# Optimization experiments

Hardware: AMD Instinct MI355X
Metric: run time of the kernel (lower is better)

The kernel has to match this reference:

```python
import jax, jax.numpy as jnp
import numpy as np

STRIDE = 32
ANCHORS = np.array([[10, 13], [16, 30], [33, 23], [30, 61], [62, 45],
                    [59, 119], [116, 90], [156, 198], [373, 326]], np.float32)
ALL_ANCH = ANCHORS / STRIDE           # [9,2] anchor w,h in grid units
ANCH_MASK = [6, 7, 8]
MASKED_ANCH = ALL_ANCH[ANCH_MASK]     # [3,2]
N_CLASSES = 80
N_ANCHORS = 3
IGNORE_THRE = 0.5


def _bce_sum(p, t, w=1.0):
    # torch BCELoss(sum): clamps log terms at -100 to avoid 0*inf
    lp = jnp.maximum(jnp.log(p), -100.0)
    lq = jnp.maximum(jnp.log(1.0 - p), -100.0)
    return jnp.sum(-w * (t * lp + (1.0 - t) * lq))


def _iou_xywh(a, b):
    # a: [B,N,4], b: [B,K,4] in (cx,cy,w,h) -> IoU [B,N,K]
    tl = jnp.maximum(a[:, :, None, :2] - a[:, :, None, 2:] / 2,
                     b[:, None, :, :2] - b[:, None, :, 2:] / 2)
    br = jnp.minimum(a[:, :, None, :2] + a[:, :, None, 2:] / 2,
                     b[:, None, :, :2] + b[:, None, :, 2:] / 2)
    en = jnp.all(tl < br, axis=-1).astype(a.dtype)
    inter = jnp.prod(br - tl, axis=-1) * en
    area_a = a[:, :, 2] * a[:, :, 3]
    area_b = b[:, :, 2] * b[:, :, 3]
    return inter / (area_a[:, :, None] + area_b[:, None, :] - inter)


def setup_inputs() -> dict:
    key = jax.random.key(0)
    k1, k2, k3, k4 = jax.random.split(key, 4)
    B, M, F, A, NC = 128, 60, 19, 3, 80
    output = jax.random.normal(k1, (B, A * (5 + NC), F, F), jnp.float32)
    cxy = jax.random.uniform(k2, (B, M, 2), jnp.float32, 100.0, 500.0)
    wh = jax.random.uniform(k3, (B, M, 2), jnp.float32, 64.0, 192.0)
    cls = jax.random.randint(k4, (B, M, 1), 0, NC).astype(jnp.float32)
    labels = jnp.concatenate([cxy - wh / 2, cxy + wh / 2, cls], axis=-1)
    return {"output": output, "labels": labels}


def reference(output, labels):
    B = output.shape[0]
    F = output.shape[2]
    n_ch = 5 + N_CLASSES
    labels = jax.lax.stop_gradient(labels)  # torch detaches labels

    # [B, A, F, F, n_ch]; sigmoid on x,y,obj,cls; raw on w,h
    out = output.reshape(B, N_ANCHORS, n_ch, F, F).transpose(0, 1, 3, 4, 2)
    out = jnp.concatenate([jax.nn.sigmoid(out[..., :2]), out[..., 2:4],
                           jax.nn.sigmoid(out[..., 4:])], axis=-1)

    # decoded pred boxes (grid units), detached as in torch (.data)
    xs = jnp.arange(F, dtype=out.dtype)
    wa = jnp.asarray(MASKED_ANCH[:, 0])[None, :, None, None]
    ha = jnp.asarray(MASKED_ANCH[:, 1])[None, :, None, None]
    px = out[..., 0] + xs[None, None, None, :]
    py = out[..., 1] + xs[None, None, :, None]
    pw = jnp.exp(out[..., 2]) * wa
    ph = jnp.exp(out[..., 3]) * ha
    pred = jax.lax.stop_gradient(jnp.stack([px, py, pw, ph], axis=-1))

    valid = labels.sum(axis=2) > 0                               # [B,M]
    tx = jnp.floor(labels[..., 0] / STRIDE)
    ty = jnp.floor(labels[..., 1] / STRIDE)
    tw = jnp.floor((labels[..., 2] - labels[..., 0]) / STRIDE)
    th = jnp.floor((labels[..., 3] - labels[..., 1]) / STRIDE)
    ti = tx.astype(jnp.int32)
    tj = ty.astype(jnp.int32)

    # anchor matching: IoU of (0,0,w,h) truths vs (0,0,aw,ah) ref anchors
    ref_wh = jnp.asarray(ALL_ANCH)                               # [9,2]
    mw = jnp.minimum(tw[..., None], ref_wh[:, 0])
    mh = jnp.minimum(th[..., None], ref_wh[:, 1])
    en = ((mw > 0) & (mh > 0)).astype(out.dtype)
    inter = mw * mh * en
    aiou = inter / (tw[..., None] * th[..., None]
                    + ref_wh[:, 0] * ref_wh[:, 1] - inter)       # [B,M,9]
    best_all = jnp.argmax(aiou, axis=-1)                         # [B,M]
    best_n = best_all % 3
    best_mask = best_all >= ANCH_MASK[0]

    # ignore mask from pred-vs-truth IoU
    truth_box = jnp.stack([tx, ty, tw, th], axis=-1)             # [B,M,4]
    ious = _iou_xywh(pred.reshape(B, -1, 4), truth_box)          # [B,AFF,M]
    ious = ious * valid[:, None, :].astype(out.dtype)
    best_iou = ious.max(axis=-1)
    obj_mask = (best_iou <= IGNORE_THRE).astype(out.dtype).reshape(B, N_ANCHORS, F, F)

    # scatter matched truths into (b, a, j, i) cells
    matched = valid & best_mask                                  # [B,M]
    NT = B * N_ANCHORS * F * F
    b_idx = jnp.broadcast_to(jnp.arange(B, dtype=jnp.int32)[:, None], matched.shape)
    flat = ((b_idx * N_ANCHORS + best_n.astype(jnp.int32)) * F + tj) * F + ti
    flat = jnp.where(matched, flat, NT).reshape(-1)              # NT is OOB -> dropped

    obj_mask = obj_mask.reshape(-1).at[flat].set(1.0, mode='drop').reshape(B, N_ANCHORS, F, F)
    tgt_mask = jnp.zeros((NT, 4 + N_CLASSES), out.dtype).at[flat].set(1.0, mode='drop')
    tgt_mask = tgt_mask.reshape(B, N_ANCHORS, F, F, 4 + N_CLASSES)

    txf = tx - tx.astype(jnp.int32).astype(out.dtype)   # exactly 0 (as in torch)
    tyf = ty - ty.astype(jnp.int32).astype(out.dtype)
    anch = jnp.asarray(MASKED_ANCH)[best_n]                      # [B,M,2]
    twt = jnp.log(tw / anch[..., 0] + 1e-16)
    tht = jnp.log(th / anch[..., 1] + 1e-16)
    onehot = jax.nn.one_hot(labels[..., 4].astype(jnp.int32), N_CLASSES, dtype=out.dtype)
    trow = jnp.concatenate([txf[..., None], tyf[..., None], twt[..., None],
                            tht[..., None], jnp.ones_like(txf)[..., None],
                            onehot], axis=-1).reshape(-1, n_ch)
    target = jnp.zeros((NT, n_ch), out.dtype).at[flat].set(trow, mode='drop')
    target = target.reshape(B, N_ANCHORS, F, F, n_ch)

    scale_val = jnp.sqrt(2.0 - tw * th / (F * F))                # [B,M]
    srow = jnp.broadcast_to(scale_val[..., None], scale_val.shape + (2,)).reshape(-1, 2)
    tgt_scale = jnp.zeros((NT, 2), out.dtype).at[flat].set(srow, mode='drop')
    tgt_scale = tgt_scale.reshape(B, N_ANCHORS, F, F, 2)

    # apply masks (in-place multiplies in torch)
    out_xy = out[..., :2] * tgt_mask[..., :2]
    out_wh = out[..., 2:4] * tgt_mask[..., 2:4] * tgt_scale
    out_obj = out[..., 4] * obj_mask
    out_cls = out[..., 5:] * tgt_mask[..., 4:]
    tgt_xy = target[..., :2] * tgt_mask[..., :2]
    tgt_wh = target[..., 2:4] * tgt_mask[..., 2:4] * tgt_scale
    tgt_obj = target[..., 4] * obj_mask
    tgt_cls = target[..., 5:] * tgt_mask[..., 4:]

    loss_xy = _bce_sum(out_xy, tgt_xy, tgt_scale * tgt_scale)
    loss_wh = 0.5 * jnp.sum((out_wh - tgt_wh) ** 2)
    loss_obj = _bce_sum(out_obj, tgt_obj)
    loss_cls = _bce_sum(out_cls, tgt_cls)
    out_full = jnp.concatenate([out_xy, out_wh, out_obj[..., None], out_cls], axis=-1)
    tgt_full = jnp.concatenate([tgt_xy, tgt_wh, tgt_obj[..., None], tgt_cls], axis=-1)
    loss_l2 = jnp.sum((out_full - tgt_full) ** 2)
    loss = loss_xy + loss_wh + loss_obj + loss_cls
    return (loss, loss_xy, loss_wh, loss_obj, loss_cls, loss_l2)
```

## Files before the change

### kernel.cpp

```cpp
#include <hip/hip_runtime.h>

#define NB 128
#define NM 60
#define NF 19
#define NA 3
#define NCELL (NF*NF)
#define NCH 85
#define NCHTOT (NA*NCH)
#define HALFC 192
#define TPB 384
#define NWAVE (TPB/64)
#define NBLK (NB*NA*2)

__device__ __constant__ float c_aw[9] = {0.3125f, 0.5f, 1.03125f, 0.9375f, 1.9375f, 1.84375f, 3.625f, 4.875f, 11.65625f};
__device__ __constant__ float c_ah[9] = {0.40625f, 0.9375f, 0.71875f, 1.90625f, 1.40625f, 3.71875f, 2.8125f, 6.1875f, 10.1875f};

__device__ __forceinline__ float clog(float v) { return fmaxf(__logf(v), -100.0f); }
__device__ __forceinline__ float sigm(float x) { return 1.0f / (1.0f + __expf(-x)); }

__device__ __forceinline__ float wave_sum(float v) {
    for (int off = 32; off > 0; off >>= 1) v += __shfl_down(v, off, 64);
    return v;
}

__global__ __launch_bounds__(TPB) void k_main(const float* __restrict__ out,
                                              const float* __restrict__ labels,
                                              float* __restrict__ partial) {
    __shared__ float4 s_box[NM];
    __shared__ float  s_ar[NM];
    __shared__ float  s_scale[NM], s_twt[NM], s_tht[NM], s_txf[NM], s_tyf[NM];
    __shared__ int    s_cls[NM];
    __shared__ int    s_win[NCELL];
    __shared__ float  s_hi[HALFC];
    __shared__ int    s_list[64];
    __shared__ int    s_n;
    __shared__ float  s_red[NWAVE][5];

    const int blk  = blockIdx.x;
    const int ba   = blk >> 1;
    const int half = blk & 1;
    const int b = ba / NA, a = ba % NA;
    const int tid = threadIdx.x;
    const int grp   = (tid >= HALFC) ? 1 : 0;
    const int local = tid - grp * HALFC;
    const int cell  = half * HALFC + local;
    const bool active = cell < NCELL;

    const float* obase = out + ((size_t)b * NCHTOT + a * NCH) * NCELL;
    float r0 = 0.f, r1 = 0.f, r2 = 0.f, r3 = 0.f, r4 = 0.f;
    if (active) {
        r0 = obase[0 * NCELL + cell];
        r1 = obase[1 * NCELL + cell];
        r2 = obase[2 * NCELL + cell];
        r3 = obase[3 * NCELL + cell];
        if (grp == 0) r4 = obase[4 * NCELL + cell];
    }

    for (int c = tid; c < NCELL; c += TPB) s_win[c] = -1;
    if (tid == 0) s_n = 0;

    if (tid < NM) {
        const float* l = labels + ((size_t)b * NM + tid) * 5;
        float x1 = l[0], y1 = l[1], x2 = l[2], y2 = l[3], cf = l[4];
        bool valid = (x1 + y1 + x2 + y2 + cf) > 0.0f;
        float tx = floorf(x1 * 0.03125f);
        float ty = floorf(y1 * 0.03125f);
        float tw = floorf((x2 - x1) * 0.03125f);
        float th = floorf((y2 - y1) * 0.03125f);
        int ti = (int)tx, tj = (int)ty;
        float bst = -1.0f; int bi = 0;
        #pragma unroll
        for (int q = 0; q < 9; q++) {
            float mw = fminf(tw, c_aw[q]), mh = fminf(th, c_ah[q]);
            float inter = (mw > 0.0f && mh > 0.0f) ? mw * mh : 0.0f;
            float iou = inter / (tw * th + c_aw[q] * c_ah[q] - inter);
            if (iou > bst) { bst = iou; bi = q; }
        }
        int bn = bi % 3;
        s_box[tid] = valid ? make_float4(tx - 0.5f * tw, ty - 0.5f * th,
                                         tx + 0.5f * tw, ty + 0.5f * th)
                           : make_float4(3.0e8f, 3.0e8f, 3.0e8f, 3.0e8f);
        s_ar[tid]    = tw * th;
        s_scale[tid] = sqrtf(2.0f - tw * th * (1.0f / (float)NCELL));
        s_twt[tid]   = __logf(tw / c_aw[6 + bn] + 1e-16f);
        s_tht[tid]   = __logf(th / c_ah[6 + bn] + 1e-16f);
        s_txf[tid]   = tx - (float)ti;
        s_tyf[tid]   = ty - (float)tj;
        s_cls[tid]   = (int)cf;
        if (valid && bi >= 6 && bn == a &&
            ti >= 0 && ti < NF && tj >= 0 && tj < NF) {
            atomicMax(&s_win[tj * NF + ti], tid);
        }
    }
    __syncthreads();

    int ii = cell % NF, jj = cell / NF;
    float sx = sigm(r0), sy = sigm(r1), sobj = sigm(r4);
    float pw = __expf(r2) * c_aw[6 + a], ph = __expf(r3) * c_ah[6 + a];
    float px = sx + (float)ii, py = sy + (float)jj;
    float px1 = px - 0.5f * pw, px2 = px + 0.5f * pw;
    float py1 = py - 0.5f * ph, py2 = py + 0.5f * ph;
    float parea = pw * ph;

    float best = 0.0f;
    const int mstart = grp * (NM / 2);
    #pragma unroll 5
    for (int m = mstart; m < mstart + NM / 2; m++) {
        float4 tb = s_box[m];
        float dx = fminf(px2, tb.z) - fmaxf(px1, tb.x);
        float dy = fminf(py2, tb.w) - fmaxf(py1, tb.y);
        float inter = fmaxf(dx, 0.0f) * fmaxf(dy, 0.0f);
        best = fmaxf(best, inter * __frcp_rn(parea + s_ar[m] - inter));
    }
    if (grp == 1) s_hi[local] = best;
    __syncthreads();

    float lxy = 0.f, lwh = 0.f, lobj = 0.f, lcls = 0.f, ll2 = 0.f;
    if (grp == 0 && active) {
        best = fmaxf(best, s_hi[local]);
        int w = s_win[cell];
        if (w >= 0) {
            float s = s_scale[w], s2 = s * s;
            float txf = s_txf[w], tyf = s_tyf[w];
            float dw = r2 - s_twt[w], dh = r3 - s_tht[w];
            lxy = -s2 * (txf * clog(sx) + (1.0f - txf) * clog(1.0f - sx)
                       + tyf * clog(sy) + (1.0f - tyf) * clog(1.0f - sy));
            float whsq = s2 * (dw * dw + dh * dh);
            lwh = 0.5f * whsq;
            lobj = -clog(sobj);
            ll2 = (sx - txf) * (sx - txf) + (sy - tyf) * (sy - tyf)
                + whsq + (sobj - 1.0f) * (sobj - 1.0f);
            int pos = atomicAdd(&s_n, 1);
            s_list[pos] = cell | (s_cls[w] << 16);
        } else if (best <= 0.5f) {
            lobj = -clog(1.0f - sobj);
            ll2 = sobj * sobj;
        }
    }
    __syncthreads();

    int nlist = s_n;
    int lane = tid & 63, wid = tid >> 6;
    for (int e = wid; e < nlist; e += NWAVE) {
        int packed = s_list[e];
        int mc = packed & 0xFFFF, k = packed >> 16;
        const float* p = obase + (size_t)5 * NCELL + mc;
        {
            float sc = sigm(p[(size_t)lane * NCELL]);
            bool isk = (lane == k);
            lcls -= isk ? clog(sc) : clog(1.0f - sc);
            float d = isk ? (sc - 1.0f) : sc;
            ll2 += d * d;
        }
        if (lane < 16) {
            int c2 = lane + 64;
            float sc = sigm(p[(size_t)c2 * NCELL]);
            bool isk = (c2 == k);
            lcls -= isk ? clog(sc) : clog(1.0f - sc);
            float d = isk ? (sc - 1.0f) : sc;
            ll2 += d * d;
        }
    }

    float v0 = wave_sum(lxy), v1 = wave_sum(lwh), v2 = wave_sum(lobj);
    float v3 = wave_sum(lcls), v4 = wave_sum(ll2);
    if (lane == 0) {
        s_red[wid][0] = v0; s_red[wid][1] = v1; s_red[wid][2] = v2;
        s_red[wid][3] = v3; s_red[wid][4] = v4;
    }
    __syncthreads();
    if (tid < 5) {
        float s = 0.0f;
        #pragma unroll
        for (int wv = 0; wv < NWAVE; wv++) s += s_red[wv][tid];
        partial[(size_t)blk * 5 + tid] = s;
    }
}

__global__ __launch_bounds__(256) void k_reduce(const float* __restrict__ partial,
                                                float* __restrict__ res) {
    __shared__ float s[4][5];
    int tid = threadIdx.x;
    float acc[5] = {0.f, 0.f, 0.f, 0.f, 0.f};
    for (int i = tid; i < NBLK; i += 256) {
        const float* p = partial + (size_t)i * 5;
        acc[0] += p[0]; acc[1] += p[1]; acc[2] += p[2];
        acc[3] += p[3]; acc[4] += p[4];
    }
    #pragma unroll
    for (int j = 0; j < 5; j++) acc[j] = wave_sum(acc[j]);
    int lane = tid & 63, wid = tid >> 6;
    if (lane == 0) {
        #pragma unroll
        for (int j = 0; j < 5; j++) s[wid][j] = acc[j];
    }
    __syncthreads();
    if (tid == 0) {
        float t[5];
        #pragma unroll
        for (int j = 0; j < 5; j++) t[j] = s[0][j] + s[1][j] + s[2][j] + s[3][j];
        res[0] = t[0] + t[1] + t[2] + t[3];
        res[1] = t[0]; res[2] = t[1]; res[3] = t[2];
        res[4] = t[3]; res[5] = t[4];
    }
}

extern "C" void kernel_launch(void* const* d_in, const int* in_sizes, int n_in,
                              void* d_out, int out_size, void* d_ws, size_t ws_size,
                              hipStream_t stream) {
    (void)in_sizes; (void)n_in; (void)out_size; (void)ws_size;
    const float* output = (const float*)d_in[0];
    const float* labels = (const float*)d_in[1];
    float* res = (float*)d_out;
    float* partial = (float*)d_ws;

    k_main<<<NBLK, TPB, 0, stream>>>(output, labels, partial);
    k_reduce<<<1, 256, 0, stream>>>(partial, res);
}
```

Before: 96.96 us.

## Fuse final reduction into main kernel via ticket and use division-free ignore test

Removes the separate reduce kernel launch. Each block writes its partial sums and takes an atomic ticket, and the last block to finish performs the global reduction, with a memset of the ticket added before launch. The ignore test now compares 3*inter > union-sum instead of computing IoU with a reciprocal, and passes only a boolean between the two thread groups. Invalid labels get a huge area so they can never trigger the ignore test. An extra __syncthreads is also added after s_win initialization.

```diff
diff --git a/kernel.cpp b/kernel.cpp
--- a/kernel.cpp
+++ b/kernel.cpp
@@ -25,15 +25,18 @@
 
 __global__ __launch_bounds__(TPB) void k_main(const float* __restrict__ out,
                                               const float* __restrict__ labels,
-                                              float* __restrict__ partial) {
+                                              float* __restrict__ partial,
+                                              int* __restrict__ ticket,
+                                              float* __restrict__ res) {
     __shared__ float4 s_box[NM];
     __shared__ float  s_ar[NM];
     __shared__ float  s_scale[NM], s_twt[NM], s_tht[NM], s_txf[NM], s_tyf[NM];
     __shared__ int    s_cls[NM];
     __shared__ int    s_win[NCELL];
-    __shared__ float  s_hi[HALFC];
+    __shared__ int    s_ign[HALFC];
     __shared__ int    s_list[64];
     __shared__ int    s_n;
+    __shared__ int    s_last;
     __shared__ float  s_red[NWAVE][5];
 
     const int blk  = blockIdx.x;
@@ -58,6 +61,7 @@
 
     for (int c = tid; c < NCELL; c += TPB) s_win[c] = -1;
     if (tid == 0) s_n = 0;
+    __syncthreads();
 
     if (tid < NM) {
         const float* l = labels + ((size_t)b * NM + tid) * 5;
@@ -80,7 +84,7 @@
         s_box[tid] = valid ? make_float4(tx - 0.5f * tw, ty - 0.5f * th,
                                          tx + 0.5f * tw, ty + 0.5f * th)
                            : make_float4(3.0e8f, 3.0e8f, 3.0e8f, 3.0e8f);
-        s_ar[tid]    = tw * th;
+        s_ar[tid]    = valid ? tw * th : 1.0e30f;
         s_scale[tid] = sqrtf(2.0f - tw * th * (1.0f / (float)NCELL));
         s_twt[tid]   = __logf(tw / c_aw[6 + bn] + 1e-16f);
         s_tht[tid]   = __logf(th / c_ah[6 + bn] + 1e-16f);
@@ -102,22 +106,22 @@
     float py1 = py - 0.5f * ph, py2 = py + 0.5f * ph;
     float parea = pw * ph;
 
-    float best = 0.0f;
+    bool ign = false;
     const int mstart = grp * (NM / 2);
-    #pragma unroll 5
+    #pragma unroll 6
     for (int m = mstart; m < mstart + NM / 2; m++) {
         float4 tb = s_box[m];
         float dx = fminf(px2, tb.z) - fmaxf(px1, tb.x);
         float dy = fminf(py2, tb.w) - fmaxf(py1, tb.y);
         float inter = fmaxf(dx, 0.0f) * fmaxf(dy, 0.0f);
-        best = fmaxf(best, inter * __frcp_rn(parea + s_ar[m] - inter));
-    }
-    if (grp == 1) s_hi[local] = best;
+        ign = ign || (3.0f * inter > parea + s_ar[m]);
+    }
+    if (grp == 1) s_ign[local] = ign ? 1 : 0;
     __syncthreads();
 
     float lxy = 0.f, lwh = 0.f, lobj = 0.f, lcls = 0.f, ll2 = 0.f;
     if (grp == 0 && active) {
-        best = fmaxf(best, s_hi[local]);
+        ign = ign || (s_ign[local] != 0);
         int w = s_win[cell];
         if (w >= 0) {
             float s = s_scale[w], s2 = s * s;
@@ -132,7 +136,7 @@
                 + whsq + (sobj - 1.0f) * (sobj - 1.0f);
             int pos = atomicAdd(&s_n, 1);
             s_list[pos] = cell | (s_cls[w] << 16);
-        } else if (best <= 0.5f) {
+        } else if (!ign) {
             lobj = -clog(1.0f - sobj);
             ll2 = sobj * sobj;
         }
@@ -169,39 +173,48 @@
         s_red[wid][3] = v3; s_red[wid][4] = v4;
     }
     __syncthreads();
-    if (tid < 5) {
-        float s = 0.0f;
+    if (tid == 0) {
+        float t0 = 0.f, t1 = 0.f, t2 = 0.f, t3 = 0.f, t4 = 0.f;
         #pragma unroll
-        for (int wv = 0; wv < NWAVE; wv++) s += s_red[wv][tid];
-        partial[(size_t)blk * 5 + tid] = s;
-    }
-}
-
-__global__ __launch_bounds__(256) void k_reduce(const float* __restrict__ partial,
-                                                float* __restrict__ res) {
-    __shared__ float s[4][5];
-    int tid = threadIdx.x;
-    float acc[5] = {0.f, 0.f, 0.f, 0.f, 0.f};
-    for (int i = tid; i < NBLK; i += 256) {
-        const float* p = partial + (size_t)i * 5;
-        acc[0] += p[0]; acc[1] += p[1]; acc[2] += p[2];
-        acc[3] += p[3]; acc[4] += p[4];
-    }
-    #pragma unroll
-    for (int j = 0; j < 5; j++) acc[j] = wave_sum(acc[j]);
-    int lane = tid & 63, wid = tid >> 6;
-    if (lane == 0) {
-        #pragma unroll
-        for (int j = 0; j < 5; j++) s[wid][j] = acc[j];
-    }
-    __syncthreads();
-    if (tid == 0) {
-        float t[5];
-        #pragma unroll
-        for (int j = 0; j < 5; j++) t[j] = s[0][j] + s[1][j] + s[2][j] + s[3][j];
-        res[0] = t[0] + t[1] + t[2] + t[3];
-        res[1] = t[0]; res[2] = t[1]; res[3] = t[2];
-        res[4] = t[3]; res[5] = t[4];
+        for (int wv = 0; wv < NWAVE; wv++) {
+            t0 += s_red[wv][0]; t1 += s_red[wv][1]; t2 += s_red[wv][2];
+            t3 += s_red[wv][3]; t4 += s_red[wv][4];
+        }
+        float* pb = partial + (size_t)blk * 5;
+        pb[0] = t0; pb[1] = t1; pb[2] = t2; pb[3] = t3; pb[4] = t4;
+        __threadfence();
+        int old = __hip_atomic_fetch_add(ticket, 1, __ATOMIC_ACQ_REL,
+                                         __HIP_MEMORY_SCOPE_AGENT);
+        s_last = (old == NBLK - 1) ? 1 : 0;
+    }
+    __syncthreads();
+    if (s_last) {
+        __threadfence();
+        float a0 = 0.f, a1 = 0.f, a2 = 0.f, a3 = 0.f, a4 = 0.f;
+        for (int i = tid; i < NBLK; i += TPB) {
+            const float* p = partial + (size_t)i * 5;
+            a0 += p[0]; a1 += p[1]; a2 += p[2]; a3 += p[3]; a4 += p[4];
+        }
+        a0 = wave_sum(a0); a1 = wave_sum(a1); a2 = wave_sum(a2);
+        a3 = wave_sum(a3); a4 = wave_sum(a4);
+        if (lane == 0) {
+            s_red[wid][0] = a0; s_red[wid][1] = a1; s_red[wid][2] = a2;
+            s_red[wid][3] = a3; s_red[wid][4] = a4;
+        }
+        __syncthreads();
+        if (tid == 0) {
+            float t[5];
+            #pragma unroll
+            for (int j = 0; j < 5; j++) {
+                float s = 0.f;
+                #pragma unroll
+                for (int wv = 0; wv < NWAVE; wv++) s += s_red[wv][j];
+                t[j] = s;
+            }
+            res[0] = t[0] + t[1] + t[2] + t[3];
+            res[1] = t[0]; res[2] = t[1]; res[3] = t[2];
+            res[4] = t[3]; res[5] = t[4];
+        }
     }
 }
 
@@ -212,8 +225,9 @@
     const float* output = (const float*)d_in[0];
     const float* labels = (const float*)d_in[1];
     float* res = (float*)d_out;
-    float* partial = (float*)d_ws;
-
-    k_main<<<NBLK, TPB, 0, stream>>>(output, labels, partial);
-    k_reduce<<<1, 256, 0, stream>>>(partial, res);
+    int*   ticket  = (int*)d_ws;
+    float* partial = (float*)((char*)d_ws + 64);
+
+    hipMemsetAsync(ticket, 0, sizeof(int), stream);
+    k_main<<<NBLK, TPB, 0, stream>>>(output, labels, partial, ticket, res);
 }
```

New measurement: 135.4 us. 39.6% more time.
